# Kernel tuning notes

Measured on AMD Instinct MI355X. Metric: run time of the kernel, lower is better.

The kernel has to match this reference:

```python
import jax, jax.numpy as jnp
import numpy as np

N_TEXT = 80000
N_NON = 20000
N = N_TEXT + N_NON
E = 200000
EMB = 256
HID = 256
R = 500
V = 17
MDIM = 64
K = 4
NUM_ROUNDS = 2
NUM_REV_ROUNDS = 2


def setup_inputs():
    key = jax.random.key(0)
    ks = jax.random.split(key, 32)
    f = jnp.float32
    s = 0.05
    inp = {}
    inp["h_id_tensor"] = jax.random.randint(ks[0], (E,), 0, N)
    inp["r_id_tensor"] = jax.random.randint(ks[1], (E,), 0, R)
    inp["t_id_tensor"] = jax.random.randint(ks[2], (E,), 0, N)
    inp["q_emb"] = jax.random.normal(ks[3], (1, EMB), f)
    inp["entity_embs"] = jax.random.normal(ks[4], (N_TEXT, EMB), f)
    inp["num_non_text_entities"] = N_NON
    inp["relation_embs"] = jax.random.normal(ks[5], (R, EMB), f)
    inp["topic_entity_one_hot"] = (jax.random.uniform(ks[6], (N, 2)) < 0.01).astype(f)
    inp["node_motif_token_ids"] = jax.random.randint(ks[7], (N, K), 0, V)
    inp["node_motif_token_wts"] = jax.random.uniform(ks[8], (N, K), f)
    inp["triple_motif_token_ids"] = jax.random.randint(ks[9], (E, K), 0, V)
    inp["triple_motif_token_wts"] = jax.random.uniform(ks[10], (E, K), f)
    inp["non_text_emb"] = jax.random.normal(ks[11], (EMB,), f) * s
    me = jax.random.normal(ks[12], (V, MDIM), f) * s
    inp["motif_emb"] = me.at[0].set(0.0)  # padding_idx=0
    inp["gnn_self_w"] = jax.random.normal(ks[13], (MDIM, MDIM), f) * s
    inp["gnn_self_b"] = jnp.zeros((MDIM,), f)
    inp["gnn_msg_w"] = jax.random.normal(ks[14], (MDIM, MDIM), f) * s
    inp["gnn_msg_b"] = jnp.zeros((MDIM,), f)
    pos_dim = 2 + 2 * (NUM_ROUNDS + NUM_REV_ROUNDS)  # 10
    inp["nh_w"] = jax.random.normal(ks[15], (2 * EMB + 2 * MDIM, HID), f) * s
    inp["nh_b"] = jnp.zeros((HID,), f)
    inp["pos_w"] = jax.random.normal(ks[16], (2 * pos_dim, HID), f) * s
    inp["pos_b"] = jnp.zeros((HID,), f)
    inp["st_w"] = jax.random.normal(ks[17], (EMB + MDIM, HID), f) * s
    inp["st_b"] = jnp.zeros((HID,), f)
    inp["gate_w"] = jax.random.normal(ks[18], (EMB, 3), f) * s
    inp["gate_b"] = jnp.zeros((3,), f)
    inp["pred_w1"] = jax.random.normal(ks[19], (EMB + HID, HID), f) * s
    inp["pred_b1"] = jnp.zeros((HID,), f)
    inp["pred_w2"] = jax.random.normal(ks[20], (HID, 1), f) * s
    inp["pred_b2"] = jnp.zeros((1,), f)
    return inp


def _forward(h_id, r_id, t_id, q_emb, entity_embs, num_non_text, relation_embs,
             topic_oh, node_ids, node_wts, trip_ids, trip_wts,
             non_text_emb, motif_emb, gsw, gsb, gmw, gmb,
             nh_w, nh_b, pos_w, pos_b, st_w, st_b, gate_w, gate_b,
             pw1, pb1, pw2, pb2):
    n = entity_embs.shape[0] + num_non_text
    h_e = jnp.concatenate(
        [entity_embs,
         jnp.broadcast_to(non_text_emb[None, :], (num_non_text, entity_embs.shape[1]))],
        axis=0)  # [N, EMB]
    ones = jnp.ones((h_id.shape[0],), h_e.dtype)
    inv_fwd = 1.0 / jnp.clip(jax.ops.segment_sum(ones, t_id, num_segments=n), 1.0)[:, None]
    inv_rev = 1.0 / jnp.clip(jax.ops.segment_sum(ones, h_id, num_segments=n), 1.0)[:, None]

    def mean_agg(x, src, dst, inv):
        # PyG mean aggregation: mean of source features over incoming edges, 0 if none
        return jax.ops.segment_sum(x[src], dst, num_segments=n) * inv

    dde_list = []
    h = topic_oh
    for _ in range(NUM_ROUNDS):
        h = mean_agg(h, h_id, t_id, inv_fwd)
        dde_list.append(h)
    h = topic_oh
    for _ in range(NUM_REV_ROUNDS):
        h = mean_agg(h, t_id, h_id, inv_rev)
        dde_list.append(h)

    # ---- motif co-occurrence adjacency (vectorized form of the K x K loop) ----
    contrib = trip_wts[:, :, None] * trip_wts[:, None, :]                 # [E,K,K]
    valid = (trip_ids[:, :, None] > 0) & (trip_ids[:, None, :] > 0) & (contrib > 0)
    contrib = jnp.where(valid, contrib, 0.0)
    idx = (trip_ids[:, :, None] * V + trip_ids[:, None, :]).reshape(-1)
    adj = jnp.zeros((V * V,), contrib.dtype).at[idx].add(contrib.reshape(-1)).reshape(V, V)
    adj = 0.5 * (adj + adj.T) + jnp.eye(V, dtype=adj.dtype)
    adj = adj.at[0, :].set(0.0).at[:, 0].set(0.0).at[0, 0].set(1.0)
    adj = adj / jnp.clip(adj.sum(axis=1, keepdims=True), 1e-8)

    # ---- semantic GNN over the motif table ----
    ht = motif_emb
    for _ in range(1):  # semantic_gnn_num_layers = 1, dropout 0 (eval)
        msg = adj @ ht
        ht = ht + jax.nn.relu(ht @ gsw + gsb + msg @ gmw + gmb)

    node_motif_emb = (ht[node_ids] * node_wts[:, :, None]).sum(axis=1)    # [N,MDIM]
    triple_motif_emb = (ht[trip_ids] * trip_wts[:, :, None]).sum(axis=1)  # [E,MDIM]

    h_r = relation_embs[r_id]                                             # [E,EMB]
    h_nbr = jax.nn.relu(
        jnp.concatenate([h_e[h_id], h_e[t_id], node_motif_emb[h_id], node_motif_emb[t_id]],
                        axis=1) @ nh_w + nh_b)
    pos_feat = jnp.concatenate([topic_oh] + dde_list, axis=1)             # [N,10]
    h_pos = jax.nn.relu(
        jnp.concatenate([pos_feat[h_id], pos_feat[t_id]], axis=1) @ pos_w + pos_b)
    h_str = jax.nn.relu(jnp.concatenate([h_r, triple_motif_emb], axis=1) @ st_w + st_b)

    gate = jax.nn.softmax((q_emb @ gate_w + gate_b)[0])                   # [3]
    h_fused = gate[0] * h_nbr + gate[1] * h_pos + gate[2] * h_str
    pred_in = jnp.concatenate(
        [jnp.broadcast_to(q_emb, (h_r.shape[0], q_emb.shape[1])), h_fused], axis=1)
    return jax.nn.relu(pred_in @ pw1 + pb1) @ pw2 + pb2                   # [E,1]


def reference(h_id_tensor, r_id_tensor, t_id_tensor, q_emb, entity_embs,
              num_non_text_entities, relation_embs, topic_entity_one_hot,
              node_motif_token_ids, node_motif_token_wts,
              triple_motif_token_ids, triple_motif_token_wts,
              non_text_emb, motif_emb, gnn_self_w, gnn_self_b, gnn_msg_w, gnn_msg_b,
              nh_w, nh_b, pos_w, pos_b, st_w, st_b, gate_w, gate_b,
              pred_w1, pred_b1, pred_w2, pred_b2):
    return _forward(h_id_tensor, r_id_tensor, t_id_tensor, q_emb, entity_embs,
                    num_non_text_entities, relation_embs, topic_entity_one_hot,
                    node_motif_token_ids, node_motif_token_wts,
                    triple_motif_token_ids, triple_motif_token_wts,
                    non_text_emb, motif_emb, gnn_self_w, gnn_self_b, gnn_msg_w, gnn_msg_b,
                    nh_w, nh_b, pos_w, pos_b, st_w, st_b, gate_w, gate_b,
                    pred_w1, pred_b1, pred_w2, pred_b2)
```

## Files before the change

### kernel.cpp

```cpp
#include <hip/hip_runtime.h>
#include <hip/hip_bf16.h>

#define N_TEXT 80000
#define NTOT   100000
#define NE     200000
#define EMB    256
#define HID    256
#define VMOT   17
#define MDIM   64
#define KTOK   4

typedef unsigned short u16;
typedef unsigned int   u32;
typedef short short8 __attribute__((ext_vector_type(8)));
typedef float f32x4 __attribute__((ext_vector_type(4)));

#define O_INVF 0
#define O_INVR (NTOT)
#define O_POS  (2*NTOT)
#define O_ADJ  (12*NTOT)
#define O_HTB  (12*NTOT + 512)
#define O_GATE (12*NTOT + 1088)
#define O_CVEC (12*NTOT + 1104)
#define O_NME  (12*NTOT + 1360)
#define O_WSW  (O_NME + NTOT*32)
#define ZERO_FLOATS (12*NTOT + 512)
#define Z4 (ZERO_FLOATS/4)

#define OW_A 0
#define OW_B 163840
#define OW_C 172032
#define OW_D 253952
#define GA 20480
#define GB 1024
#define GC 10240
#define GD 8192
#define GTOT (GA+GB+GC+GD)

__device__ __forceinline__ u16 f2b(float f) {
  unsigned u = __float_as_uint(f);
  return (u16)((u + 0x7fffu + ((u >> 16) & 1u)) >> 16);
}
__device__ __forceinline__ float b2f(u16 v) {
  return __uint_as_float(((unsigned)v) << 16);
}
__device__ __forceinline__ short8 pack8f(const float* f) {
  union { u32 u[4]; short8 s; } o;
#pragma unroll
  for (int i = 0; i < 4; i++) {
    __hip_bfloat162 b = __float22bfloat162_rn(float2{f[2*i], f[2*i+1]});
    o.u[i] = *reinterpret_cast<u32*>(&b);
  }
  return o.s;
}

__global__ void k_prep(const float* __restrict__ nh_w, const float* __restrict__ pos_w,
                       const float* __restrict__ st_w, const float* __restrict__ pw1,
                       float* __restrict__ ws) {
  int g = blockIdx.x * blockDim.x + threadIdx.x;
  if (g < Z4) { ((float4*)ws)[g] = make_float4(0.f, 0.f, 0.f, 0.f); return; }
  g -= Z4;
  if (g >= GTOT) return;
  int l, phase;
  if (g < GA) { l = g; phase = 0; }
  else if (g < GA + GB) { l = g - GA; phase = 1; }
  else if (g < GA + GB + GC) { l = g - GA - GB; phase = 2; }
  else { l = g - GA - GB - GC; phase = 3; }
  int c = l >> 10, r = l & 1023;
  int w = r >> 8, nt = (r >> 6) & 3, ln = r & 63;
  int col = w*64 + nt*16 + (ln & 15);
  int k0  = c*32 + ((ln >> 4) << 3);
  float f[8];
#pragma unroll
  for (int j = 0; j < 8; j++) {
    int k = k0 + j;
    float v = 0.f;
    if (phase == 0)      v = nh_w[k*256 + col];
    else if (phase == 1) { if (k < 10) v = pos_w[k*256 + col];
                           else if (k >= 16 && k < 26) v = pos_w[(k-6)*256 + col]; }
    else if (phase == 2) v = st_w[k*256 + col];
    else                 v = pw1[(256 + k)*256 + col];
    f[j] = v;
  }
  ((short8*)((u16*)(ws + O_WSW)))[g] = pack8f(f);
}

__global__ void k_deg_dde1_adj(const int* __restrict__ h_id, const int* __restrict__ t_id,
                               const float* __restrict__ topic,
                               const int* __restrict__ tids, const float* __restrict__ twts,
                               float* __restrict__ ws) {
  __shared__ float sadj[4*304];
  for (int i = threadIdx.x; i < 4*304; i += blockDim.x) sadj[i] = 0.f;
  __syncthreads();
  int wbase = (threadIdx.x >> 6) * 304;
  int e = blockIdx.x * blockDim.x + threadIdx.x;
  if (e < NE) {
    int h = h_id[e], t = t_id[e];
    atomicAdd(&ws[O_INVF + t], 1.0f);
    atomicAdd(&ws[O_INVR + h], 1.0f);
    float hx = topic[2*h], hy = topic[2*h + 1];
    float tx = topic[2*t], ty = topic[2*t + 1];
    if (hx != 0.f) atomicAdd(&ws[O_POS + t*10 + 2], hx);
    if (hy != 0.f) atomicAdd(&ws[O_POS + t*10 + 3], hy);
    if (tx != 0.f) atomicAdd(&ws[O_POS + h*10 + 6], tx);
    if (ty != 0.f) atomicAdd(&ws[O_POS + h*10 + 7], ty);
    int id[KTOK]; float w[KTOK];
#pragma unroll
    for (int k = 0; k < KTOK; k++) { id[k] = tids[e*KTOK + k]; w[k] = twts[e*KTOK + k]; }
#pragma unroll
    for (int i = 0; i < KTOK; i++)
#pragma unroll
      for (int j = 0; j < KTOK; j++) {
        float c = w[i] * w[j];
        if (id[i] > 0 && id[j] > 0 && c > 0.f)
          atomicAdd(&sadj[wbase + id[i]*VMOT + id[j]], c);
      }
  }
  __syncthreads();
  for (int i = threadIdx.x; i < VMOT*VMOT; i += blockDim.x) {
    float v = sadj[i] + sadj[304 + i] + sadj[608 + i] + sadj[912 + i];
    if (v != 0.f) atomicAdd(&ws[O_ADJ + i], v);
  }
}

#define NPN_BLOCKS ((NTOT + 255)/256)
__global__ void k_pnm(const float* __restrict__ topic, const float* __restrict__ mo,
                      const float* __restrict__ gsw, const float* __restrict__ gsb,
                      const float* __restrict__ gmw, const float* __restrict__ gmb,
                      const float* __restrict__ q, const float* __restrict__ gate_w,
                      const float* __restrict__ gate_b, const float* __restrict__ pw1,
                      const float* __restrict__ pb1, float* __restrict__ ws) {
  int t = threadIdx.x;
  if (blockIdx.x < NPN_BLOCKS) {
    int n = blockIdx.x * 256 + t;
    if (n >= NTOT) return;
    float invf = 1.0f / fmaxf(ws[O_INVF + n], 1.0f);
    float invr = 1.0f / fmaxf(ws[O_INVR + n], 1.0f);
    ws[O_INVF + n] = invf;
    ws[O_INVR + n] = invr;
    float* p = &ws[O_POS + n*10];
    p[0] = topic[2*n]; p[1] = topic[2*n + 1];
    p[2] *= invf; p[3] *= invf;
    p[6] *= invr; p[7] *= invr;
  } else if (blockIdx.x == NPN_BLOCKS) {
    __shared__ float A[VMOT*VMOT];
    __shared__ float Bm[VMOT*VMOT];
    __shared__ float inv_row[VMOT];
    __shared__ float smo[VMOT*MDIM];
    __shared__ float sm[VMOT*MDIM];
    for (int i = t; i < VMOT*VMOT; i += 256) A[i] = ws[O_ADJ + i];
    for (int i = t; i < VMOT*MDIM; i += 256) smo[i] = mo[i];
    __syncthreads();
    for (int i = t; i < VMOT*VMOT; i += 256) {
      int r = i / VMOT, c = i % VMOT;
      float v = 0.5f * (A[i] + A[c*VMOT + r]) + (r == c ? 1.f : 0.f);
      if (r == 0 || c == 0) v = (r == 0 && c == 0) ? 1.f : 0.f;
      Bm[i] = v;
    }
    __syncthreads();
    if (t < VMOT) {
      float s = 0.f;
      for (int c = 0; c < VMOT; c++) s += Bm[t*VMOT + c];
      inv_row[t] = 1.f / fmaxf(s, 1e-8f);
    }
    __syncthreads();
    for (int i = t; i < VMOT*MDIM; i += 256) {
      int v = i / MDIM, d = i % MDIM;
      float s = 0.f;
      for (int u = 0; u < VMOT; u++) s += Bm[v*VMOT + u] * smo[u*MDIM + d];
      sm[i] = s * inv_row[v];
    }
    __syncthreads();
    for (int i = t; i < VMOT*MDIM; i += 256) {
      int v = i / MDIM, d = i % MDIM;
      float a = gsb[d] + gmb[d];
      for (int m = 0; m < MDIM; m++)
        a += smo[v*MDIM + m] * gsw[m*MDIM + d] + sm[v*MDIM + m] * gmw[m*MDIM + d];
      ((u16*)(ws + O_HTB))[i] = f2b(smo[i] + fmaxf(a, 0.f));
    }
  } else {
    __shared__ float sq[EMB];
    __shared__ float red[3];
    sq[t] = q[t];
    if (t < 3) red[t] = 0.f;
    __syncthreads();
    float s = pb1[t];
    for (int i = 0; i < EMB; i++) s += sq[i] * pw1[i*HID + t];
    ws[O_CVEC + t] = s;
    atomicAdd(&red[0], sq[t] * gate_w[t*3 + 0]);
    atomicAdd(&red[1], sq[t] * gate_w[t*3 + 1]);
    atomicAdd(&red[2], sq[t] * gate_w[t*3 + 2]);
    __syncthreads();
    if (t == 0) {
      float l0 = red[0] + gate_b[0], l1 = red[1] + gate_b[1], l2 = red[2] + gate_b[2];
      float mx = fmaxf(l0, fmaxf(l1, l2));
      float e0 = expf(l0 - mx), e1 = expf(l1 - mx), e2 = expf(l2 - mx);
      float inv = 1.f / (e0 + e1 + e2);
      ws[O_GATE + 0] = e0 * inv; ws[O_GATE + 1] = e1 * inv; ws[O_GATE + 2] = e2 * inv;
    }
  }
}

__global__ void k_dde2(const int* __restrict__ h_id, const int* __restrict__ t_id,
                       float* __restrict__ ws) {
  int e = blockIdx.x * blockDim.x + threadIdx.x;
  if (e >= NE) return;
  int h = h_id[e], t = t_id[e];
  float a = ws[O_POS + h*10 + 2], b = ws[O_POS + h*10 + 3];
  float c = ws[O_POS + t*10 + 6], d = ws[O_POS + t*10 + 7];
  if (a != 0.f) atomicAdd(&ws[O_POS + t*10 + 4], a);
  if (b != 0.f) atomicAdd(&ws[O_POS + t*10 + 5], b);
  if (c != 0.f) atomicAdd(&ws[O_POS + h*10 + 8], c);
  if (d != 0.f) atomicAdd(&ws[O_POS + h*10 + 9], d);
}

__global__ void k_scale_nme(const int* __restrict__ nids, const float* __restrict__ nwts,
                            float* __restrict__ ws) {
  __shared__ u16 sht[VMOT*MDIM];
  for (int i = threadIdx.x; i < (VMOT*MDIM)/2; i += blockDim.x)
    ((u32*)sht)[i] = ((const u32*)(ws + O_HTB))[i];
  __syncthreads();
  int gid = blockIdx.x * blockDim.x + threadIdx.x;
  if (gid < NTOT) {
    float invf = ws[O_INVF + gid], invr = ws[O_INVR + gid];
    float* p = &ws[O_POS + gid*10];
    p[4] *= invf; p[5] *= invf;
    p[8] *= invr; p[9] *= invr;
  }
  if (gid >= NTOT * 8) return;
  int n = gid >> 3, d0 = (gid & 7) * 8;
  int4   iv = ((const int4*)nids)[n];
  float4 wv = ((const float4*)nwts)[n];
  float f[8];
#pragma unroll
  for (int j = 0; j < 8; j++) {
    f[j] = wv.x * b2f(sht[iv.x*MDIM + d0 + j]) + wv.y * b2f(sht[iv.y*MDIM + d0 + j])
         + wv.z * b2f(sht[iv.z*MDIM + d0 + j]) + wv.w * b2f(sht[iv.w*MDIM + d0 + j]);
  }
  ((short8*)((u16*)(ws + O_NME)))[gid] = pack8f(f);
}

__global__ __launch_bounds__(256, 4) void k_edge_mfma(
    const int* __restrict__ h_id, const int* __restrict__ r_id, const int* __restrict__ t_id,
    const float* __restrict__ ent, const float* __restrict__ rel, const float* __restrict__ nte,
    const int* __restrict__ tids, const float* __restrict__ twts,
    const float* __restrict__ nh_b, const float* __restrict__ pos_b,
    const float* __restrict__ st_b, const float* __restrict__ pw2,
    const float* __restrict__ pb2,
    const float* __restrict__ ws, float* __restrict__ out) {
  __shared__ __align__(16) u16 sX[64*32];
  __shared__ __align__(16) u16 sF[16384];
  __shared__ float sOut[64];
  __shared__ int sh[64], stt[64], sr[64];

  const int tid = threadIdx.x;
  const int wv = tid >> 6, ln = tid & 63;
  const int lm = ln & 15, lq = ln >> 4;
  const int cb = wv * 64;
  const int e0 = blockIdx.x * 64;
  const int srow = tid >> 2, sks = tid & 3;

  if (tid < 64) {
    sh[tid]  = h_id[e0 + tid];
    stt[tid] = t_id[e0 + tid];
    sr[tid]  = r_id[e0 + tid];
    sOut[tid] = 0.f;
  }
  const float g0 = ws[O_GATE + 0], g1 = ws[O_GATE + 1], g2 = ws[O_GATE + 2];
  const u16* blob = (const u16*)(ws + O_WSW);
  const u16* nmeb = (const u16*)(ws + O_NME);
  const u16* htb  = (const u16*)(ws + O_HTB);
  const int4   tiv = ((const int4*)tids)[e0 + srow];
  const float4 twv = ((const float4*)twts)[e0 + srow];
  __syncthreads();

  f32x4 acc[4][4];
#pragma unroll
  for (int mt = 0; mt < 4; mt++)
#pragma unroll
    for (int nt = 0; nt < 4; nt++) acc[mt][nt] = (f32x4){0.f, 0.f, 0.f, 0.f};

#define MFMA_STEP(bc)                                                    \
  { short8 a[4], b[4];                                                   \
    _Pragma("unroll")                                                    \
    for (int nt = 0; nt < 4; nt++)                                       \
      b[nt] = *(const short8*)&blob[(bc)*8192 + wv*2048 + nt*512 + ln*8];\
    _Pragma("unroll")                                                    \
    for (int mt = 0; mt < 4; mt++)                                       \
      a[mt] = *(const short8*)&sX[(mt*16 + lm)*32 + lq*8];               \
    _Pragma("unroll")                                                    \
    for (int mt = 0; mt < 4; mt++)                                       \
      _Pragma("unroll")                                                  \
      for (int nt = 0; nt < 4; nt++)                                     \
        acc[mt][nt] = __builtin_amdgcn_mfma_f32_16x16x32_bf16(a[mt], b[nt], acc[mt][nt], 0, 0, 0); }

  {
    float4 fa, fb; short8 xs;
    auto loadA = [&](int kc) {
      int kk = kc + sks*8;
      if (kk < 512) {
        int node = (kk < 256) ? sh[srow] : stt[srow];
        int k2 = kk & 255;
        const float* src = (node < N_TEXT) ? &ent[(size_t)node*256 + k2] : &nte[k2];
        fa = *(const float4*)src; fb = *(const float4*)(src + 4);
      } else {
        int node = (kk < 576) ? sh[srow] : stt[srow];
        xs = *(const short8*)&nmeb[(size_t)node*64 + ((kk - 512) & 63)];
      }
    };
    loadA(0);
#pragma unroll 2
    for (int c = 0; c < 20; c++) {
      if (c < 16) {
        float f[8] = {fa.x, fa.y, fa.z, fa.w, fb.x, fb.y, fb.z, fb.w};
        *(short8*)&sX[srow*32 + sks*8] = pack8f(f);
      } else {
        *(short8*)&sX[srow*32 + sks*8] = xs;
      }
      __syncthreads();
      if (c < 19) loadA((c+1)*32);
      MFMA_STEP(c);
      __syncthreads();
    }
  }
#pragma unroll
  for (int nt = 0; nt < 4; nt++) {
    int col = cb + nt*16 + lm;
    float bb = nh_b[col];
    int base = (col >> 5)*2048 + (col & 31);
#pragma unroll
    for (int mt = 0; mt < 4; mt++)
#pragma unroll
      for (int r = 0; r < 4; r++) {
        sF[base + (mt*16 + lq*4 + r)*32] = f2b(g0 * fmaxf(acc[mt][nt][r] + bb, 0.f));
        acc[mt][nt][r] = 0.f;
      }
  }

  {
    int node_h = sh[srow], node_t = stt[srow];
    float f[8];
#pragma unroll
    for (int j = 0; j < 8; j++) {
      int kk = sks*8 + j;
      float v = 0.f;
      if (kk < 10) v = ws[O_POS + (size_t)node_h*10 + kk];
      else if (kk >= 16 && kk < 26) v = ws[O_POS + (size_t)node_t*10 + kk - 16];
      f[j] = v;
    }
    *(short8*)&sX[srow*32 + sks*8] = pack8f(f);
    __syncthreads();
    MFMA_STEP(20);
    __syncthreads();
  }
#pragma unroll
  for (int nt = 0; nt < 4; nt++) {
    int col = cb + nt*16 + lm;
    float bb = pos_b[col];
    int base = (col >> 5)*2048 + (col & 31);
#pragma unroll
    for (int mt = 0; mt < 4; mt++)
#pragma unroll
      for (int r = 0; r < 4; r++) {
        u16* p = &sF[base + (mt*16 + lq*4 + r)*32];
        *p = f2b(b2f(*p) + g1 * fmaxf(acc[mt][nt][r] + bb, 0.f));
        acc[mt][nt][r] = 0.f;
      }
  }

  {
    float4 fa, fb; short8 hs0, hs1, hs2, hs3;
    auto loadC = [&](int kc) {
      int kk = kc + sks*8;
      if (kk < 256) {
        const float* src = &rel[(size_t)sr[srow]*256 + kk];
        fa = *(const float4*)src; fb = *(const float4*)(src + 4);
      } else {
        int d0 = kk - 256;
        hs0 = *(const short8*)&htb[tiv.x*64 + d0];
        hs1 = *(const short8*)&htb[tiv.y*64 + d0];
        hs2 = *(const short8*)&htb[tiv.z*64 + d0];
        hs3 = *(const short8*)&htb[tiv.w*64 + d0];
      }
    };
    loadC(0);
#pragma unroll 2
    for (int c = 0; c < 10; c++) {
      if (c < 8) {
        float f[8] = {fa.x, fa.y, fa.z, fa.w, fb.x, fb.y, fb.z, fb.w};
        *(short8*)&sX[srow*32 + sks*8] = pack8f(f);
      } else {
        float f[8];
#pragma unroll
        for (int j = 0; j < 8; j++)
          f[j] = twv.x * b2f((u16)hs0[j]) + twv.y * b2f((u16)hs1[j])
               + twv.z * b2f((u16)hs2[j]) + twv.w * b2f((u16)hs3[j]);
        *(short8*)&sX[srow*32 + sks*8] = pack8f(f);
      }
      __syncthreads();
      if (c < 9) loadC((c+1)*32);
      MFMA_STEP(21 + c);
      __syncthreads();
    }
  }
#pragma unroll
  for (int nt = 0; nt < 4; nt++) {
    int col = cb + nt*16 + lm;
    float bb = st_b[col];
    int base = (col >> 5)*2048 + (col & 31);
#pragma unroll
    for (int mt = 0; mt < 4; mt++)
#pragma unroll
      for (int r = 0; r < 4; r++) {
        u16* p = &sF[base + (mt*16 + lq*4 + r)*32];
        *p = f2b(b2f(*p) + g2 * fmaxf(acc[mt][nt][r] + bb, 0.f));
        acc[mt][nt][r] = 0.f;
      }
  }

  __syncthreads();

#pragma unroll 2
  for (int c = 0; c < 8; c++) {
    short8 a[4], b[4];
#pragma unroll
    for (int nt = 0; nt < 4; nt++)
      b[nt] = *(const short8*)&blob[(31 + c)*8192 + wv*2048 + nt*512 + ln*8];
#pragma unroll
    for (int mt = 0; mt < 4; mt++)
      a[mt] = *(const short8*)&sF[c*2048 + (mt*16 + lm)*32 + lq*8];
#pragma unroll
    for (int mt = 0; mt < 4; mt++)
#pragma unroll
      for (int nt = 0; nt < 4; nt++)
        acc[mt][nt] = __builtin_amdgcn_mfma_f32_16x16x32_bf16(a[mt], b[nt], acc[mt][nt], 0, 0, 0);
  }

  {
    float cv[4], p2[4];
#pragma unroll
    for (int nt = 0; nt < 4; nt++) {
      int col = cb + nt*16 + lm;
      cv[nt] = ws[O_CVEC + col];
      p2[nt] = pw2[col];
    }
#pragma unroll
    for (int mt = 0; mt < 4; mt++)
#pragma unroll
      for (int r = 0; r < 4; r++) {
        float s = 0.f;
#pragma unroll
        for (int nt = 0; nt < 4; nt++)
          s += fmaxf(acc[mt][nt][r] + cv[nt], 0.f) * p2[nt];
#pragma unroll
        for (int off = 1; off < 16; off <<= 1)
          s += __shfl_xor(s, off, 64);
        if (lm == 0) atomicAdd(&sOut[mt*16 + lq*4 + r], s);
      }
  }
  __syncthreads();
  if (tid < 64) out[e0 + tid] = sOut[tid] + pb2[0];
#undef MFMA_STEP
}

extern "C" void kernel_launch(void* const* d_in, const int* in_sizes, int n_in,
                              void* d_out, int out_size, void* d_ws, size_t ws_size,
                              hipStream_t stream) {
  (void)in_sizes; (void)n_in; (void)out_size; (void)ws_size;
  const int*   h_id   = (const int*)  d_in[0];
  const int*   r_id   = (const int*)  d_in[1];
  const int*   t_id   = (const int*)  d_in[2];
  const float* q      = (const float*)d_in[3];
  const float* ent    = (const float*)d_in[4];
  const float* rel    = (const float*)d_in[6];
  const float* topic  = (const float*)d_in[7];
  const int*   nids   = (const int*)  d_in[8];
  const float* nwts   = (const float*)d_in[9];
  const int*   tids   = (const int*)  d_in[10];
  const float* twts   = (const float*)d_in[11];
  const float* nte    = (const float*)d_in[12];
  const float* mo     = (const float*)d_in[13];
  const float* gsw    = (const float*)d_in[14];
  const float* gsb    = (const float*)d_in[15];
  const float* gmw    = (const float*)d_in[16];
  const float* gmb    = (const float*)d_in[17];
  const float* nh_w   = (const float*)d_in[18];
  const float* nh_b   = (const float*)d_in[19];
  const float* pos_w  = (const float*)d_in[20];
  const float* pos_b  = (const float*)d_in[21];
  const float* st_w   = (const float*)d_in[22];
  const float* st_b   = (const float*)d_in[23];
  const float* gate_w = (const float*)d_in[24];
  const float* gate_b = (const float*)d_in[25];
  const float* pw1    = (const float*)d_in[26];
  const float* pb1    = (const float*)d_in[27];
  const float* pw2    = (const float*)d_in[28];
  const float* pb2    = (const float*)d_in[29];
  float* ws  = (float*)d_ws;
  float* out = (float*)d_out;

  k_prep<<<(Z4 + GTOT + 255)/256, 256, 0, stream>>>(nh_w, pos_w, st_w, pw1, ws);
  k_deg_dde1_adj<<<(NE + 255)/256, 256, 0, stream>>>(h_id, t_id, topic, tids, twts, ws);
  k_pnm<<<NPN_BLOCKS + 2, 256, 0, stream>>>(topic, mo, gsw, gsb, gmw, gmb,
                                            q, gate_w, gate_b, pw1, pb1, ws);
  k_dde2<<<(NE + 255)/256, 256, 0, stream>>>(h_id, t_id, ws);
  k_scale_nme<<<(NTOT*8 + 255)/256, 256, 0, stream>>>(nids, nwts, ws);
  k_edge_mfma<<<NE/64, 256, 0, stream>>>(h_id, r_id, t_id, ent, rel, nte, tids, twts,
                                         nh_b, pos_b, st_b, pw2, pb2, ws, out);
}
```

Measured before the change: 475.4 us.

## Double-buffer LDS A tiles, swizzle layout to MFMA order, drop index staging

Replaces the single sX staging tile with two buffers so each K-step needs one barrier instead of two, storing the next chunk while MFMAs consume the current one. Rewrites the sX and sF layouts into MFMA fragment order (lane-contiguous 16-byte reads) to avoid LDS bank conflicts. Loads edge indices straight into registers rather than through shared memory, reuses sF for the output reduction, and moves the weighted motif sum into the load stage. It adds register pressure and more complex buffer bookkeeping.

New measurement: 495.0 us. 1.04x slower.

```diff
diff --git a/kernel.cpp b/kernel.cpp
--- a/kernel.cpp
+++ b/kernel.cpp
@@ -27,10 +27,6 @@
 #define ZERO_FLOATS (12*NTOT + 512)
 #define Z4 (ZERO_FLOATS/4)
 
-#define OW_A 0
-#define OW_B 163840
-#define OW_C 172032
-#define OW_D 253952
 #define GA 20480
 #define GB 1024
 #define GC 10240
@@ -248,10 +244,8 @@
     const float* __restrict__ st_b, const float* __restrict__ pw2,
     const float* __restrict__ pb2,
     const float* __restrict__ ws, float* __restrict__ out) {
-  __shared__ __align__(16) u16 sX[64*32];
+  __shared__ __align__(16) u16 sX[2][2048];
   __shared__ __align__(16) u16 sF[16384];
-  __shared__ float sOut[64];
-  __shared__ int sh[64], stt[64], sr[64];
 
   const int tid = threadIdx.x;
   const int wv = tid >> 6, ln = tid & 63;
@@ -259,20 +253,18 @@
   const int cb = wv * 64;
   const int e0 = blockIdx.x * 64;
   const int srow = tid >> 2, sks = tid & 3;
-
-  if (tid < 64) {
-    sh[tid]  = h_id[e0 + tid];
-    stt[tid] = t_id[e0 + tid];
-    sr[tid]  = r_id[e0 + tid];
-    sOut[tid] = 0.f;
-  }
+  const int xoff = (srow >> 4)*512 + (sks*16 + (srow & 15))*8;
+
+  const int   hS = h_id[e0 + srow];
+  const int   tS = t_id[e0 + srow];
+  const int   rS = r_id[e0 + srow];
+  const int4   tivS = ((const int4*)tids)[e0 + srow];
+  const float4 twvS = ((const float4*)twts)[e0 + srow];
+
   const float g0 = ws[O_GATE + 0], g1 = ws[O_GATE + 1], g2 = ws[O_GATE + 2];
   const u16* blob = (const u16*)(ws + O_WSW);
   const u16* nmeb = (const u16*)(ws + O_NME);
   const u16* htb  = (const u16*)(ws + O_HTB);
-  const int4   tiv = ((const int4*)tids)[e0 + srow];
-  const float4 twv = ((const float4*)twts)[e0 + srow];
-  __syncthreads();
 
   f32x4 acc[4][4];
 #pragma unroll
@@ -280,139 +272,139 @@
 #pragma unroll
     for (int nt = 0; nt < 4; nt++) acc[mt][nt] = (f32x4){0.f, 0.f, 0.f, 0.f};
 
-#define MFMA_STEP(bc)                                                    \
+#define MFMA_STEP(buf, bc)                                               \
   { short8 a[4], b[4];                                                   \
     _Pragma("unroll")                                                    \
     for (int nt = 0; nt < 4; nt++)                                       \
       b[nt] = *(const short8*)&blob[(bc)*8192 + wv*2048 + nt*512 + ln*8];\
     _Pragma("unroll")                                                    \
     for (int mt = 0; mt < 4; mt++)                                       \
-      a[mt] = *(const short8*)&sX[(mt*16 + lm)*32 + lq*8];               \
+      a[mt] = *(const short8*)&sX[buf][mt*512 + ln*8];                   \
     _Pragma("unroll")                                                    \
     for (int mt = 0; mt < 4; mt++)                                       \
       _Pragma("unroll")                                                  \
       for (int nt = 0; nt < 4; nt++)                                     \
         acc[mt][nt] = __builtin_amdgcn_mfma_f32_16x16x32_bf16(a[mt], b[nt], acc[mt][nt], 0, 0, 0); }
 
-  {
-    float4 fa, fb; short8 xs;
-    auto loadA = [&](int kc) {
-      int kk = kc + sks*8;
-      if (kk < 512) {
-        int node = (kk < 256) ? sh[srow] : stt[srow];
-        int k2 = kk & 255;
-        const float* src = (node < N_TEXT) ? &ent[(size_t)node*256 + k2] : &nte[k2];
-        fa = *(const float4*)src; fb = *(const float4*)(src + 4);
-      } else {
-        int node = (kk < 576) ? sh[srow] : stt[srow];
-        xs = *(const short8*)&nmeb[(size_t)node*64 + ((kk - 512) & 63)];
+
+  float4 fa, fb; short8 xs;
+  auto loadA = [&](int c) {
+    int kk = c*32 + sks*8;
+    if (kk < 512) {
+      int node = (kk < 256) ? hS : tS;
+      int k2 = kk & 255;
+      const float* src = (node < N_TEXT) ? &ent[(size_t)node*256 + k2] : &nte[k2];
+      fa = *(const float4*)src; fb = *(const float4*)(src + 4);
+    } else {
+      int node = (kk < 576) ? hS : tS;
+      xs = *(const short8*)&nmeb[(size_t)node*64 + ((kk - 512) & 63)];
+    }
+  };
+  auto storeA = [&](int buf, int c) {
+    if (c < 16) {
+      float f[8] = {fa.x, fa.y, fa.z, fa.w, fb.x, fb.y, fb.z, fb.w};
+      *(short8*)&sX[buf][xoff] = pack8f(f);
+    } else {
+      *(short8*)&sX[buf][xoff] = xs;
+    }
+  };
+  auto loadC = [&](int c) {
+    int kk = c*32 + sks*8;
+    if (kk < 256) {
+      const float* src = &rel[(size_t)rS*256 + kk];
+      fa = *(const float4*)src; fb = *(const float4*)(src + 4);
+    } else {
+      int d0 = kk - 256;
+      short8 h0 = *(const short8*)&htb[tivS.x*64 + d0];
+      short8 h1 = *(const short8*)&htb[tivS.y*64 + d0];
+      short8 h2 = *(const short8*)&htb[tivS.z*64 + d0];
+      short8 h3 = *(const short8*)&htb[tivS.w*64 + d0];
+      float f[8];
+#pragma unroll
+      for (int j = 0; j < 8; j++)
+        f[j] = twvS.x * b2f((u16)h0[j]) + twvS.y * b2f((u16)h1[j])
+             + twvS.z * b2f((u16)h2[j]) + twvS.w * b2f((u16)h3[j]);
+      xs = pack8f(f);
+    }
+  };
+  auto storeC = [&](int buf, int c) {
+    if (c < 8) {
+      float f[8] = {fa.x, fa.y, fa.z, fa.w, fb.x, fb.y, fb.z, fb.w};
+      *(short8*)&sX[buf][xoff] = pack8f(f);
+    } else {
+      *(short8*)&sX[buf][xoff] = xs;
+    }
+  };
+
+  loadA(0); storeA(0, 0);
+  for (int c = 0; c < 20; c++) {
+    __syncthreads();
+    if (c < 19) loadA(c + 1);
+    MFMA_STEP(c & 1, c);
+    if (c < 19) {
+      storeA((c + 1) & 1, c + 1);
+    } else {
+      float f[8];
+#pragma unroll
+      for (int j = 0; j < 8; j++) {
+        int kk = sks*8 + j;
+        float v = 0.f;
+        if (kk < 10) v = ws[O_POS + (size_t)hS*10 + kk];
+        else if (kk >= 16 && kk < 26) v = ws[O_POS + (size_t)tS*10 + kk - 16];
+        f[j] = v;
       }
-    };
-    loadA(0);
-#pragma unroll 2
-    for (int c = 0; c < 20; c++) {
-      if (c < 16) {
-        float f[8] = {fa.x, fa.y, fa.z, fa.w, fb.x, fb.y, fb.z, fb.w};
-        *(short8*)&sX[srow*32 + sks*8] = pack8f(f);
-      } else {
-        *(short8*)&sX[srow*32 + sks*8] = xs;
-      }
-      __syncthreads();
-      if (c < 19) loadA((c+1)*32);
-      MFMA_STEP(c);
-      __syncthreads();
+      *(short8*)&sX[0][xoff] = pack8f(f);
     }
   }
 #pragma unroll
   for (int nt = 0; nt < 4; nt++) {
     int col = cb + nt*16 + lm;
     float bb = nh_b[col];
-    int base = (col >> 5)*2048 + (col & 31);
+    int base = (col >> 5)*2048 + ((col >> 3) & 3)*128 + (col & 7);
 #pragma unroll
     for (int mt = 0; mt < 4; mt++)
 #pragma unroll
       for (int r = 0; r < 4; r++) {
-        sF[base + (mt*16 + lq*4 + r)*32] = f2b(g0 * fmaxf(acc[mt][nt][r] + bb, 0.f));
+        sF[base + mt*512 + (lq*4 + r)*8] = f2b(g0 * fmaxf(acc[mt][nt][r] + bb, 0.f));
         acc[mt][nt][r] = 0.f;
       }
   }
 
-  {
-    int node_h = sh[srow], node_t = stt[srow];
-    float f[8];
-#pragma unroll
-    for (int j = 0; j < 8; j++) {
-      int kk = sks*8 + j;
-      float v = 0.f;
-      if (kk < 10) v = ws[O_POS + (size_t)node_h*10 + kk];
-      else if (kk >= 16 && kk < 26) v = ws[O_POS + (size_t)node_t*10 + kk - 16];
-      f[j] = v;
-    }
-    *(short8*)&sX[srow*32 + sks*8] = pack8f(f);
-    __syncthreads();
-    MFMA_STEP(20);
-    __syncthreads();
-  }
+  __syncthreads();
+  MFMA_STEP(0, 20);
+  loadC(0);
 #pragma unroll
   for (int nt = 0; nt < 4; nt++) {
     int col = cb + nt*16 + lm;
     float bb = pos_b[col];
-    int base = (col >> 5)*2048 + (col & 31);
+    int base = (col >> 5)*2048 + ((col >> 3) & 3)*128 + (col & 7);
 #pragma unroll
     for (int mt = 0; mt < 4; mt++)
 #pragma unroll
       for (int r = 0; r < 4; r++) {
-        u16* p = &sF[base + (mt*16 + lq*4 + r)*32];
+        u16* p = &sF[base + mt*512 + (lq*4 + r)*8];
         *p = f2b(b2f(*p) + g1 * fmaxf(acc[mt][nt][r] + bb, 0.f));
         acc[mt][nt][r] = 0.f;
       }
   }
-
-  {
-    float4 fa, fb; short8 hs0, hs1, hs2, hs3;
-    auto loadC = [&](int kc) {
-      int kk = kc + sks*8;
-      if (kk < 256) {
-        const float* src = &rel[(size_t)sr[srow]*256 + kk];
-        fa = *(const float4*)src; fb = *(const float4*)(src + 4);
-      } else {
-        int d0 = kk - 256;
-        hs0 = *(const short8*)&htb[tiv.x*64 + d0];
-        hs1 = *(const short8*)&htb[tiv.y*64 + d0];
-        hs2 = *(const short8*)&htb[tiv.z*64 + d0];
-        hs3 = *(const short8*)&htb[tiv.w*64 + d0];
-      }
-    };
-    loadC(0);
-#pragma unroll 2
-    for (int c = 0; c < 10; c++) {
-      if (c < 8) {
-        float f[8] = {fa.x, fa.y, fa.z, fa.w, fb.x, fb.y, fb.z, fb.w};
-        *(short8*)&sX[srow*32 + sks*8] = pack8f(f);
-      } else {
-        float f[8];
-#pragma unroll
-        for (int j = 0; j < 8; j++)
-          f[j] = twv.x * b2f((u16)hs0[j]) + twv.y * b2f((u16)hs1[j])
-               + twv.z * b2f((u16)hs2[j]) + twv.w * b2f((u16)hs3[j]);
-        *(short8*)&sX[srow*32 + sks*8] = pack8f(f);
-      }
-      __syncthreads();
-      if (c < 9) loadC((c+1)*32);
-      MFMA_STEP(21 + c);
-      __syncthreads();
-    }
+  storeC(1, 0);
+
+  for (int c = 0; c < 10; c++) {
+    __syncthreads();
+    if (c < 9) loadC(c + 1);
+    MFMA_STEP((c + 1) & 1, 21 + c);
+    if (c < 9) storeC(c & 1, c + 1);
   }
 #pragma unroll
   for (int nt = 0; nt < 4; nt++) {
     int col = cb + nt*16 + lm;
     float bb = st_b[col];
-    int base = (col >> 5)*2048 + (col & 31);
+    int base = (col >> 5)*2048 + ((col >> 3) & 3)*128 + (col & 7);
 #pragma unroll
     for (int mt = 0; mt < 4; mt++)
 #pragma unroll
       for (int r = 0; r < 4; r++) {
-        u16* p = &sF[base + (mt*16 + lq*4 + r)*32];
+        u16* p = &sF[base + mt*512 + (lq*4 + r)*8];
         *p = f2b(b2f(*p) + g2 * fmaxf(acc[mt][nt][r] + bb, 0.f));
         acc[mt][nt][r] = 0.f;
       }
@@ -428,7 +420,7 @@
       b[nt] = *(const short8*)&blob[(31 + c)*8192 + wv*2048 + nt*512 + ln*8];
 #pragma unroll
     for (int mt = 0; mt < 4; mt++)
-      a[mt] = *(const short8*)&sF[c*2048 + (mt*16 + lm)*32 + lq*8];
+      a[mt] = *(const short8*)&sF[c*2048 + mt*512 + ln*8];
 #pragma unroll
     for (int mt = 0; mt < 4; mt++)
 #pragma unroll
@@ -436,6 +428,10 @@
         acc[mt][nt] = __builtin_amdgcn_mfma_f32_16x16x32_bf16(a[mt], b[nt], acc[mt][nt], 0, 0, 0);
   }
 
+  __syncthreads();
+  float* sOut = (float*)sF;
+  if (tid < 64) sOut[tid] = 0.f;
+  __syncthreads();
   {
     float cv[4], p2[4];
 #pragma unroll
```
